# Performance work log

Measured on AMD Instinct MI355X. Metric: run time of the kernel, lower is better.

The kernel has to match this reference:

```python
import jax, jax.numpy as jnp
import numpy as np

DT = 0.02
STEPS = 50          # SDE_MAX_T / SDE_DT
S = 16              # SDE_N_SIM
TEMP = 20.0
DETACH_K = 10
LATENT = 128
B = 16384


def setup_inputs() -> dict:
    key = jax.random.key(0)
    ks = jax.random.split(key, 8)
    z = jax.random.normal(ks[0], (B, LATENT), jnp.float32)
    W1 = jax.random.normal(ks[1], (64, LATENT + 2), jnp.float32) / np.sqrt(LATENT + 2)
    b1 = jnp.zeros((64,), jnp.float32)
    W2 = jax.random.normal(ks[2], (2, 64), jnp.float32) / np.sqrt(64)
    b2 = jnp.array([0.5, 0.0], jnp.float32)  # matches nn.init in _init_sde
    Wb = jax.random.normal(ks[3], (1, LATENT), jnp.float32) / np.sqrt(LATENT)
    bb = jnp.zeros((1,), jnp.float32)
    Wn = jax.random.normal(ks[4], (1, LATENT), jnp.float32) / np.sqrt(LATENT)
    bn = jnp.zeros((1,), jnp.float32)
    out_scale = jnp.array([0.001, 0.001, 0.1], jnp.float32)
    out_bias = jnp.zeros((3,), jnp.float32)
    noise = jax.random.normal(ks[5], (STEPS, B, S), jnp.float32)
    return {"z": z, "W1": W1, "b1": b1, "W2": W2, "b2": b2, "Wb": Wb, "bb": bb,
            "Wn": Wn, "bn": bn, "out_scale": out_scale, "out_bias": out_bias,
            "noise": noise}


def reference(z, W1, b1, W2, b2, Wb, bb, Wn, bn, out_scale, out_bias, noise):
    sqrt_dt = DT ** 0.5
    boundary = jax.nn.softplus(z @ Wb.T + bb)[:, 0] + 0.3   # (B,)
    ndt = jax.nn.softplus(z @ Wn.T + bn)[:, 0] + 0.05       # (B,)
    half_b = boundary * 0.5
    Bn = z.shape[0]
    z_exp = jnp.broadcast_to(z[:, None, :], (Bn, S, z.shape[1]))  # (B,S,L)

    def step(carry, xs):
        x, log_surv, exp_rt, exp_corr = carry
        k, nz = xs
        # periodic detach of the state (no-op for forward values)
        x = jnp.where((k > 0) & (k % DETACH_K == 0), jax.lax.stop_gradient(x), x)
        t_val = k.astype(x.dtype) * DT
        t_col = jnp.broadcast_to(t_val, x.shape)[..., None]          # (B,S,1)
        inp = jnp.concatenate([x[..., None], t_col, z_exp], axis=-1)  # (B,S,L+2)
        h = jnp.tanh(inp @ W1.T + b1)
        dyn = h @ W2.T + b2                                           # (B,S,2)
        drift = jnp.clip(dyn[..., 0], -5.0, 5.0)
        diff = jax.nn.softplus(dyn[..., 1]) + 0.1
        x = jnp.clip(x + drift * DT + diff * sqrt_dt * nz, -10.0, 10.0)
        dist = jnp.abs(x) - half_b[:, None]
        hazard = jnp.clip(jax.nn.sigmoid(TEMP * dist), 0.0, 0.99)
        surv_before = jnp.exp(jnp.maximum(log_surv, -50.0))
        cross_p = surv_before * hazard
        log_surv = log_surv + jnp.log1p(-hazard)
        t_now = (k + 1).astype(x.dtype) * DT
        exp_rt = exp_rt + cross_p * t_now
        exp_corr = exp_corr + cross_p * (x > 0).astype(x.dtype)
        return (x, log_surv, exp_rt, exp_corr), None

    zero = jnp.zeros((Bn, S), z.dtype)
    carry0 = (zero, zero, zero, zero)
    (x, log_surv, exp_rt, exp_corr), _ = jax.lax.scan(
        step, carry0, (jnp.arange(STEPS), noise))

    remaining = jnp.exp(jnp.maximum(log_surv, -50.0))
    exp_rt = exp_rt + remaining * (STEPS * DT)
    exp_corr = exp_corr + remaining * 0.5
    rt_ms = (exp_rt + ndt[:, None]) * 1000.0
    raw = jnp.stack([rt_ms.mean(axis=1),
                     rt_ms.std(axis=1, ddof=1) + 0.001,   # torch unbiased std
                     exp_corr.mean(axis=1)], axis=1)
    out = raw * out_scale + out_bias
    return jnp.nan_to_num(out, nan=0.0)
```

## Files before the change

### kernel.cpp

```cpp
#include <hip/hip_runtime.h>
#include <math.h>

#define SDE_B 16384
#define SDE_S 16
#define SDE_STEPS 50
#define SDE_L 128
#define SDE_DT 0.02f
#define SDE_SQRT_DT 0.14142135623730951f
#define SDE_TEMP 20.0f
#define LOG2E 1.44269504088896340736f
#define LN2 0.69314718055994530942f

typedef float f2 __attribute__((ext_vector_type(2)));

#if __has_builtin(__builtin_amdgcn_exp2f)
__device__ __forceinline__ float fexp2(float x) { return __builtin_amdgcn_exp2f(x); }
#else
__device__ __forceinline__ float fexp2(float x) { return __exp2f(x); }
#endif

#if __has_builtin(__builtin_amdgcn_logf)
__device__ __forceinline__ float flog2(float x) { return __builtin_amdgcn_logf(x); }
#else
__device__ __forceinline__ float flog2(float x) { return __log2f(x); }
#endif

#if __has_builtin(__builtin_amdgcn_rcpf)
__device__ __forceinline__ float frcp(float x) { return __builtin_amdgcn_rcpf(x); }
#else
__device__ __forceinline__ float frcp(float x) { return 1.0f / x; }
#endif

__device__ __forceinline__ f2 ffma2(f2 a, f2 b, f2 c) {
#if __has_builtin(__builtin_elementwise_fma)
    return __builtin_elementwise_fma(a, b, c);
#else
    return (f2){fmaf(a.x, b.x, c.x), fmaf(a.y, b.y, c.y)};
#endif
}
__device__ __forceinline__ f2 fclamp2(f2 v, float lo, float hi) {
#if __has_builtin(__builtin_elementwise_min) && __has_builtin(__builtin_elementwise_max)
    return __builtin_elementwise_min(__builtin_elementwise_max(v, (f2){lo, lo}), (f2){hi, hi});
#else
    return (f2){fminf(fmaxf(v.x, lo), hi), fminf(fmaxf(v.y, lo), hi)};
#endif
}

__device__ __forceinline__ float softplus_fast(float y) {
    float m = fmaxf(y, 0.0f);
    float e = fexp2(-fabsf(y) * LOG2E);
    return fmaf(LN2, flog2(1.0f + e), m);
}

__device__ __forceinline__ float sigmoid_fast(float y) {
    return frcp(1.0f + fexp2(-y * LOG2E));
}

__device__ __forceinline__ float quad_sum(float v) {
#if __has_builtin(__builtin_amdgcn_mov_dpp)
    int i = __float_as_int(v);
    v += __int_as_float(__builtin_amdgcn_mov_dpp(i, 0xB1, 0xF, 0xF, true));
    i = __float_as_int(v);
    v += __int_as_float(__builtin_amdgcn_mov_dpp(i, 0x4E, 0xF, 0xF, true));
    return v;
#else
    v += __shfl_xor(v, 1, 64);
    v += __shfl_xor(v, 2, 64);
    return v;
#endif
}

__device__ __forceinline__ float fixnum(float v) {
    if (isnan(v)) return 0.0f;
    if (isinf(v)) return v > 0.0f ? 3.4028234663852886e38f : -3.4028234663852886e38f;
    return v;
}

__global__ void __launch_bounds__(256)
__attribute__((amdgpu_waves_per_eu(4, 4))) sde_kernel(
    const float* __restrict__ z,  const float* __restrict__ W1,
    const float* __restrict__ b1, const float* __restrict__ W2,
    const float* __restrict__ b2, const float* __restrict__ Wb,
    const float* __restrict__ bb, const float* __restrict__ Wn,
    const float* __restrict__ bn, const float* __restrict__ osc,
    const float* __restrict__ obias, const float* __restrict__ noise,
    float* __restrict__ out)
{
    __shared__ float w1s[64 * 131];

    for (int idx = threadIdx.x; idx < 64 * 130; idx += 256) {
        int row = idx / 130, col = idx - row * 130;
        w1s[row * 131 + col] = W1[idx];
    }
    __syncthreads();

    const int lane = threadIdx.x & 63;
    const int wv = threadIdx.x >> 6;
    const int b = blockIdx.x * 4 + wv;
    if (b >= SDE_B) return;
    const int s = lane >> 2;
    const int q = lane & 3;

    const float* zr = z + (size_t)b * SDE_L;

    float accz = b1[lane];
    #pragma unroll
    for (int m = 0; m < SDE_L; m += 4) {
        float z0 = zr[m], z1 = zr[m + 1], z2 = zr[m + 2], z3 = zr[m + 3];
        const float* wrow = &w1s[lane * 131 + 2 + m];
        accz = fmaf(z0, wrow[0], accz);
        accz = fmaf(z1, wrow[1], accz);
        accz = fmaf(z2, wrow[2], accz);
        accz = fmaf(z3, wrow[3], accz);
    }

    float zb0 = zr[2 * lane], zb1 = zr[2 * lane + 1];
    float pb = fmaf(zb0, Wb[2 * lane], zb1 * Wb[2 * lane + 1]);
    float pn = fmaf(zb0, Wn[2 * lane], zb1 * Wn[2 * lane + 1]);
    #pragma unroll
    for (int off = 32; off > 0; off >>= 1) {
        pb += __shfl_xor(pb, off, 64);
        pn += __shfl_xor(pn, off, 64);
    }
    const float half_b = 0.5f * (softplus_fast(pb + bb[0]) + 0.3f);
    const float ndt = softplus_fast(pn + bn[0]) + 0.05f;

    f2 zw2[8], w1x2[8], w1t2[8], w2a2[8], w2b2[8];
    #pragma unroll
    for (int p = 0; p < 8; ++p) {
        int j0 = 4 * (2 * p) + q, j1 = 4 * (2 * p + 1) + q;
        zw2[p]  = (f2){__shfl(accz, j0, 64), __shfl(accz, j1, 64)};
        w1x2[p] = (f2){w1s[j0 * 131 + 0], w1s[j1 * 131 + 0]};
        w1t2[p] = (f2){w1s[j0 * 131 + 1], w1s[j1 * 131 + 1]};
        w2a2[p] = (f2){W2[j0], W2[j1]};
        w2b2[p] = (f2){W2[64 + j0], W2[64 + j1]};
    }

    const float b20 = b2[0], b21 = b2[1];
    const float* nzp = noise + (size_t)b * SDE_S + s;
    const f2 c105 = (f2){105.0f, 105.0f};
    const f2 c945 = (f2){945.0f, 945.0f};
    const f2 c15  = (f2){15.0f, 15.0f};
    const f2 c420 = (f2){420.0f, 420.0f};

    float x = 0.0f, surv = 1.0f, ert = 0.0f, ecorr = 0.0f;
    float nz = nzp[0];

    for (int k = 0; k < SDE_STEPS; ++k) {
        int kn = (k + 1 < SDE_STEPS) ? k + 1 : k;
        float nz_next = nzp[(size_t)kn * (SDE_B * SDE_S)];

        float t = (float)k * SDE_DT;
        f2 x2 = (f2){x, x}, t2 = (f2){t, t};
        f2 A0 = (f2){0.0f, 0.0f}, A1 = (f2){0.0f, 0.0f};
        #pragma unroll
        for (int g = 0; g < 4; ++g) {
            f2 pre0 = ffma2(x2, w1x2[2 * g],     ffma2(t2, w1t2[2 * g],     zw2[2 * g]));
            f2 pre1 = ffma2(x2, w1x2[2 * g + 1], ffma2(t2, w1t2[2 * g + 1], zw2[2 * g + 1]));
            pre0 = fclamp2(pre0, -3.8f, 3.8f);
            pre1 = fclamp2(pre1, -3.8f, 3.8f);
            f2 tt0 = pre0 * pre0, tt1 = pre1 * pre1;
            f2 num0 = pre0 * ffma2(tt0, tt0 + c105, c945);
            f2 num1 = pre1 * ffma2(tt1, tt1 + c105, c945);
            f2 den0 = ffma2(tt0, ffma2(tt0, c15, c420), c945);
            f2 den1 = ffma2(tt1, ffma2(tt1, c15, c420), c945);
            f2 den0s = __builtin_shufflevector(den0, den0, 1, 0);
            f2 den1s = __builtin_shufflevector(den1, den1, 1, 0);
            float p01 = den0.x * den0.y;
            float p23 = den1.x * den1.y;
            float r = frcp(p01 * p23);
            float r01 = r * p23, r23 = r * p01;
            f2 h0 = (num0 * den0s) * (f2){r01, r01};
            f2 h1 = (num1 * den1s) * (f2){r23, r23};
            A0 = ffma2(h0, w2a2[2 * g], A0);
            A0 = ffma2(h1, w2a2[2 * g + 1], A0);
            A1 = ffma2(h0, w2b2[2 * g], A1);
            A1 = ffma2(h1, w2b2[2 * g + 1], A1);
        }
        float a0 = A0.x + A0.y;
        float a1 = A1.x + A1.y;
        a0 = quad_sum(a0);
        a1 = quad_sum(a1);
        float drift = fminf(fmaxf(a0 + b20, -5.0f), 5.0f);
        float diff = softplus_fast(a1 + b21) + 0.1f;
        x = fmaf(drift, SDE_DT, fmaf(diff * SDE_SQRT_DT, nz, x));
        x = fminf(fmaxf(x, -10.0f), 10.0f);
        float dist = fabsf(x) - half_b;
        float hz = fminf(sigmoid_fast(SDE_TEMP * dist), 0.99f);
        float cross = surv * hz;
        surv = surv * (1.0f - hz);
        float tn = (float)(k + 1) * SDE_DT;
        ert = fmaf(cross, tn, ert);
        ecorr += (x > 0.0f) ? cross : 0.0f;
        nz = nz_next;
    }

    ert += surv;
    ecorr = fmaf(surv, 0.5f, ecorr);
    float rt = ert + ndt;

    float sr = (q == 0) ? rt : 0.0f;
    float scr = (q == 0) ? ecorr : 0.0f;
    #pragma unroll
    for (int off = 32; off > 0; off >>= 1) {
        sr += __shfl_xor(sr, off, 64);
        scr += __shfl_xor(scr, off, 64);
    }
    float mean = sr * (1.0f / 16.0f);
    float d = rt - mean;
    float vv = (q == 0) ? d * d : 0.0f;
    #pragma unroll
    for (int off = 32; off > 0; off >>= 1) vv += __shfl_xor(vv, off, 64);

    if (lane == 0) {
        float std_ms = sqrtf(vv * (1.0f / 15.0f)) * 1000.0f + 0.001f;
        float o0 = fmaf(mean * 1000.0f, osc[0], obias[0]);
        float o1 = fmaf(std_ms, osc[1], obias[1]);
        float o2 = fmaf(scr * (1.0f / 16.0f), osc[2], obias[2]);
        out[b * 3 + 0] = fixnum(o0);
        out[b * 3 + 1] = fixnum(o1);
        out[b * 3 + 2] = fixnum(o2);
    }
}

extern "C" void kernel_launch(void* const* d_in, const int* in_sizes, int n_in,
                              void* d_out, int out_size, void* d_ws, size_t ws_size,
                              hipStream_t stream) {
    const float* z     = (const float*)d_in[0];
    const float* W1    = (const float*)d_in[1];
    const float* b1    = (const float*)d_in[2];
    const float* W2    = (const float*)d_in[3];
    const float* b2    = (const float*)d_in[4];
    const float* Wb    = (const float*)d_in[5];
    const float* bb    = (const float*)d_in[6];
    const float* Wn    = (const float*)d_in[7];
    const float* bn    = (const float*)d_in[8];
    const float* osc   = (const float*)d_in[9];
    const float* obias = (const float*)d_in[10];
    const float* noise = (const float*)d_in[11];
    float* out = (float*)d_out;

    dim3 grid(SDE_B / 4), block(256);
    sde_kernel<<<grid, block, 0, stream>>>(z, W1, b1, W2, b2, Wb, bb, Wn, bn,
                                           osc, obias, noise, out);
}
```

Baseline: 380.6 us.

## Split each simulation across eight lanes and two waves per batch row

```diff
diff --git a/kernel.cpp b/kernel.cpp
--- a/kernel.cpp
+++ b/kernel.cpp
@@ -56,16 +56,19 @@
     return frcp(1.0f + fexp2(-y * LOG2E));
 }
 
-__device__ __forceinline__ float quad_sum(float v) {
+__device__ __forceinline__ float oct_sum(float v) {
 #if __has_builtin(__builtin_amdgcn_mov_dpp)
     int i = __float_as_int(v);
     v += __int_as_float(__builtin_amdgcn_mov_dpp(i, 0xB1, 0xF, 0xF, true));
     i = __float_as_int(v);
     v += __int_as_float(__builtin_amdgcn_mov_dpp(i, 0x4E, 0xF, 0xF, true));
+    i = __float_as_int(v);
+    v += __int_as_float(__builtin_amdgcn_mov_dpp(i, 0x141, 0xF, 0xF, true));
     return v;
 #else
     v += __shfl_xor(v, 1, 64);
     v += __shfl_xor(v, 2, 64);
+    v += __shfl_xor(v, 4, 64);
     return v;
 #endif
 }
@@ -76,8 +79,7 @@
     return v;
 }
 
-__global__ void __launch_bounds__(256)
-__attribute__((amdgpu_waves_per_eu(4, 4))) sde_kernel(
+__global__ void __launch_bounds__(256) sde_kernel(
     const float* __restrict__ z,  const float* __restrict__ W1,
     const float* __restrict__ b1, const float* __restrict__ W2,
     const float* __restrict__ b2, const float* __restrict__ Wb,
@@ -86,32 +88,27 @@
     const float* __restrict__ obias, const float* __restrict__ noise,
     float* __restrict__ out)
 {
-    __shared__ float w1s[64 * 131];
-
-    for (int idx = threadIdx.x; idx < 64 * 130; idx += 256) {
-        int row = idx / 130, col = idx - row * 130;
-        w1s[row * 131 + col] = W1[idx];
-    }
-    __syncthreads();
+    __shared__ float sm_rt[32];
+    __shared__ float sm_ec[32];
 
     const int lane = threadIdx.x & 63;
     const int wv = threadIdx.x >> 6;
-    const int b = blockIdx.x * 4 + wv;
-    if (b >= SDE_B) return;
-    const int s = lane >> 2;
-    const int q = lane & 3;
+    const int b_local = wv >> 1;
+    const int b = blockIdx.x * 2 + b_local;
+    const int o = lane & 7;
+    const int s = ((wv & 1) << 3) | (lane >> 3);
 
     const float* zr = z + (size_t)b * SDE_L;
 
     float accz = b1[lane];
-    #pragma unroll
-    for (int m = 0; m < SDE_L; m += 4) {
-        float z0 = zr[m], z1 = zr[m + 1], z2 = zr[m + 2], z3 = zr[m + 3];
-        const float* wrow = &w1s[lane * 131 + 2 + m];
-        accz = fmaf(z0, wrow[0], accz);
-        accz = fmaf(z1, wrow[1], accz);
-        accz = fmaf(z2, wrow[2], accz);
-        accz = fmaf(z3, wrow[3], accz);
+    {
+        const float* wrow = W1 + lane * 130 + 2;
+        #pragma unroll
+        for (int m = 0; m < SDE_L; m += 2) {
+            float2 w = *(const float2*)(wrow + m);
+            accz = fmaf(zr[m], w.x, accz);
+            accz = fmaf(zr[m + 1], w.y, accz);
+        }
     }
 
     float zb0 = zr[2 * lane], zb1 = zr[2 * lane + 1];
@@ -125,13 +122,15 @@
     const float half_b = 0.5f * (softplus_fast(pb + bb[0]) + 0.3f);
     const float ndt = softplus_fast(pn + bn[0]) + 0.05f;
 
-    f2 zw2[8], w1x2[8], w1t2[8], w2a2[8], w2b2[8];
+    f2 zw2[4], w1x2[4], w1t2[4], w2a2[4], w2b2[4];
     #pragma unroll
-    for (int p = 0; p < 8; ++p) {
-        int j0 = 4 * (2 * p) + q, j1 = 4 * (2 * p + 1) + q;
-        zw2[p]  = (f2){__shfl(accz, j0, 64), __shfl(accz, j1, 64)};
-        w1x2[p] = (f2){w1s[j0 * 131 + 0], w1s[j1 * 131 + 0]};
-        w1t2[p] = (f2){w1s[j0 * 131 + 1], w1s[j1 * 131 + 1]};
+    for (int p = 0; p < 4; ++p) {
+        int j0 = 16 * p + o, j1 = j0 + 8;
+        zw2[p] = (f2){__shfl(accz, j0, 64), __shfl(accz, j1, 64)};
+        float2 wa = *(const float2*)(W1 + j0 * 130);
+        float2 wb = *(const float2*)(W1 + j1 * 130);
+        w1x2[p] = (f2){wa.x, wb.x};
+        w1t2[p] = (f2){wa.y, wb.y};
         w2a2[p] = (f2){W2[j0], W2[j1]};
         w2b2[p] = (f2){W2[64 + j0], W2[64 + j1]};
     }
@@ -144,17 +143,16 @@
     const f2 c420 = (f2){420.0f, 420.0f};
 
     float x = 0.0f, surv = 1.0f, ert = 0.0f, ecorr = 0.0f;
-    float nz = nzp[0];
+    float t = 0.0f;
 
     for (int k = 0; k < SDE_STEPS; ++k) {
-        int kn = (k + 1 < SDE_STEPS) ? k + 1 : k;
-        float nz_next = nzp[(size_t)kn * (SDE_B * SDE_S)];
-
-        float t = (float)k * SDE_DT;
+        float nz = *nzp;
+        nzp += SDE_B * SDE_S;
+
         f2 x2 = (f2){x, x}, t2 = (f2){t, t};
         f2 A0 = (f2){0.0f, 0.0f}, A1 = (f2){0.0f, 0.0f};
         #pragma unroll
-        for (int g = 0; g < 4; ++g) {
+        for (int g = 0; g < 2; ++g) {
             f2 pre0 = ffma2(x2, w1x2[2 * g],     ffma2(t2, w1t2[2 * g],     zw2[2 * g]));
             f2 pre1 = ffma2(x2, w1x2[2 * g + 1], ffma2(t2, w1t2[2 * g + 1], zw2[2 * g + 1]));
             pre0 = fclamp2(pre0, -3.8f, 3.8f);
@@ -172,15 +170,11 @@
             float r01 = r * p23, r23 = r * p01;
             f2 h0 = (num0 * den0s) * (f2){r01, r01};
             f2 h1 = (num1 * den1s) * (f2){r23, r23};
-            A0 = ffma2(h0, w2a2[2 * g], A0);
-            A0 = ffma2(h1, w2a2[2 * g + 1], A0);
-            A1 = ffma2(h0, w2b2[2 * g], A1);
-            A1 = ffma2(h1, w2b2[2 * g + 1], A1);
-        }
-        float a0 = A0.x + A0.y;
-        float a1 = A1.x + A1.y;
-        a0 = quad_sum(a0);
-        a1 = quad_sum(a1);
+            A0 = ffma2(h0, w2a2[2 * g], ffma2(h1, w2a2[2 * g + 1], A0));
+            A1 = ffma2(h0, w2b2[2 * g], ffma2(h1, w2b2[2 * g + 1], A1));
+        }
+        float a0 = oct_sum(A0.x + A0.y);
+        float a1 = oct_sum(A1.x + A1.y);
         float drift = fminf(fmaxf(a0 + b20, -5.0f), 5.0f);
         float diff = softplus_fast(a1 + b21) + 0.1f;
         x = fmaf(drift, SDE_DT, fmaf(diff * SDE_SQRT_DT, nz, x));
@@ -189,37 +183,45 @@
         float hz = fminf(sigmoid_fast(SDE_TEMP * dist), 0.99f);
         float cross = surv * hz;
         surv = surv * (1.0f - hz);
-        float tn = (float)(k + 1) * SDE_DT;
-        ert = fmaf(cross, tn, ert);
+        t += SDE_DT;
+        ert = fmaf(cross, t, ert);
         ecorr += (x > 0.0f) ? cross : 0.0f;
-        nz = nz_next;
     }
 
     ert += surv;
     ecorr = fmaf(surv, 0.5f, ecorr);
     float rt = ert + ndt;
 
-    float sr = (q == 0) ? rt : 0.0f;
-    float scr = (q == 0) ? ecorr : 0.0f;
-    #pragma unroll
-    for (int off = 32; off > 0; off >>= 1) {
-        sr += __shfl_xor(sr, off, 64);
-        scr += __shfl_xor(scr, off, 64);
-    }
-    float mean = sr * (1.0f / 16.0f);
-    float d = rt - mean;
-    float vv = (q == 0) ? d * d : 0.0f;
-    #pragma unroll
-    for (int off = 32; off > 0; off >>= 1) vv += __shfl_xor(vv, off, 64);
-
-    if (lane == 0) {
-        float std_ms = sqrtf(vv * (1.0f / 15.0f)) * 1000.0f + 0.001f;
-        float o0 = fmaf(mean * 1000.0f, osc[0], obias[0]);
-        float o1 = fmaf(std_ms, osc[1], obias[1]);
-        float o2 = fmaf(scr * (1.0f / 16.0f), osc[2], obias[2]);
-        out[b * 3 + 0] = fixnum(o0);
-        out[b * 3 + 1] = fixnum(o1);
-        out[b * 3 + 2] = fixnum(o2);
+    if (o == 0) {
+        sm_rt[b_local * 16 + s] = rt;
+        sm_ec[b_local * 16 + s] = ecorr;
+    }
+    __syncthreads();
+
+    if ((wv & 1) == 0 && lane < 16) {
+        float v = sm_rt[b_local * 16 + lane];
+        float e = sm_ec[b_local * 16 + lane];
+        float sum = v, se = e;
+        #pragma unroll
+        for (int off = 8; off > 0; off >>= 1) {
+            sum += __shfl_xor(sum, off, 64);
+            se += __shfl_xor(se, off, 64);
+        }
+        float mean = sum * (1.0f / 16.0f);
+        float d = v - mean;
+        float vv = d * d;
+        #pragma unroll
+        for (int off = 8; off > 0; off >>= 1) vv += __shfl_xor(vv, off, 64);
+
+        if (lane == 0) {
+            float std_ms = sqrtf(vv * (1.0f / 15.0f)) * 1000.0f + 0.001f;
+            float o0 = fmaf(mean * 1000.0f, osc[0], obias[0]);
+            float o1 = fmaf(std_ms, osc[1], obias[1]);
+            float o2 = fmaf(se * (1.0f / 16.0f), osc[2], obias[2]);
+            out[b * 3 + 0] = fixnum(o0);
+            out[b * 3 + 1] = fixnum(o1);
+            out[b * 3 + 2] = fixnum(o2);
+        }
     }
 }
 
@@ -240,7 +242,7 @@
     const float* noise = (const float*)d_in[11];
     float* out = (float*)d_out;
 
-    dim3 grid(SDE_B / 4), block(256);
+    dim3 grid(SDE_B / 2), block(256);
     sde_kernel<<<grid, block, 0, stream>>>(z, W1, b1, W2, b2, Wb, bb, Wn, bn,
                                            osc, obias, noise, out);
 }
```

After: 431.3 us. 13.3% more time.
